# Kernel tuning notes

Hardware: AMD Instinct MI355X
Metric: run time of the kernel (lower is better)

Reference implementation:

```python
import jax, jax.numpy as jnp
import numpy as np

E = 16777216       # total edges across the batch
NG = 1024          # num_graphs
K = 32             # action_topk
TEMP = 1.0         # policy_temperature


def setup_inputs() -> dict:
    key = jax.random.key(0)
    k1, k2, k3, k4, k5 = jax.random.split(key, 5)
    edge_logits = jax.random.normal(k1, (E,), dtype=jnp.float32)
    edge_scores = jax.random.normal(k2, (E,), dtype=jnp.float32)
    stop_logits = jax.random.normal(k3, (NG,), dtype=jnp.float32)
    edge_batch = jnp.sort(jax.random.randint(k4, (E,), 0, NG)).astype(jnp.int64)
    candidate_mask = jax.random.randint(k5, (E,), 0, 2).astype(bool)
    return {
        'edge_logits': edge_logits,
        'edge_scores': edge_scores,
        'stop_logits': stop_logits,
        'edge_batch': edge_batch,
        'candidate_mask': candidate_mask,
    }


def _topk_edge_mask(edge_scores, edge_batch, candidate_mask):
    """Faithful port of _select_topk_candidate_edges, returning a boolean keep
    mask over all E edges (fixed shape; indices of kept edges are implicit)."""
    neg_inf = jnp.finfo(jnp.float32).min
    # Non-candidates get a sentinel segment NG and -inf score so they sort last.
    seg_key = jnp.where(candidate_mask, edge_batch, NG)
    score = jnp.where(candidate_mask, edge_scores.astype(jnp.float32), neg_inf)
    # Sort by score descending, then stable-sort by segment id
    order_score = jnp.argsort(-score)
    seg_by_score = seg_key[order_score]
    order_seg = jnp.argsort(seg_by_score)          # jax argsort is stable
    cand_sorted = order_score[order_seg]           # original edge ids, sorted
    seg_sorted = seg_by_score[order_seg]
    # rank within each segment = position - segment start (exclusive cumsum)
    counts = jnp.bincount(seg_sorted, length=NG + 1)
    start = jnp.concatenate([jnp.zeros((1,), counts.dtype), jnp.cumsum(counts)[:-1]])
    rank = jnp.arange(E) - start[seg_sorted]
    keep_sorted = (rank < K) & (seg_sorted < NG)
    return jnp.zeros((E,), dtype=bool).at[cand_sorted].set(keep_sorted)


def _segment_logsumexp_1d(logits, segment_ids, num_segments):
    """Faithful port of torch _segment_logsumexp_1d."""
    neg_inf = jnp.finfo(logits.dtype).min
    eps = jnp.finfo(logits.dtype).eps
    max_per = jnp.full((num_segments,), neg_inf, dtype=logits.dtype).at[segment_ids].max(logits)
    exp = jnp.exp(logits - max_per[segment_ids])
    sum_per = jnp.zeros((num_segments,), dtype=logits.dtype).at[segment_ids].add(exp)
    return jnp.log(jnp.maximum(sum_per, eps)) + max_per


def reference(edge_logits, edge_scores, stop_logits, edge_batch, candidate_mask):
    neg_inf = jnp.finfo(jnp.float32).min
    # Per-graph top-k pruning of candidate edges by edge_scores
    valid = _topk_edge_mask(edge_scores, edge_batch, candidate_mask)
    # Segmented temperature softmax over (valid edges + stop action)
    logits_t = edge_logits / TEMP
    stop_t = stop_logits / TEMP
    masked = jnp.where(valid, logits_t, neg_inf)
    lse_edges = _segment_logsumexp_1d(masked, edge_batch, NG)       # [NG]
    log_denom = jnp.logaddexp(lse_edges, stop_t)                    # [NG]
    log_prob_edge = jnp.where(valid, logits_t - log_denom[edge_batch], neg_inf)
    return log_prob_edge
```

## Files before the change

kernel.cpp:

```cpp
#include <hip/hip_runtime.h>
#include <float.h>

#define TPB  512
#define KTOP 32
#define GCAP 512
#define LCAP 1024
#define SENT_U32 0xFF7F0000u
#define VCLAMP 3.0e38f
#define STHRESH 2.0f

__device__ __forceinline__ unsigned int f2u(float f){
  unsigned int u = __float_as_uint(f);
  return (u & 0x80000000u) ? ~u : (u | 0x80000000u);
}

__device__ int suffix_total(int* hist, int NB, int* gsum, int tid){
  int GS = NB >> 8;
  if (tid < 256){
    int p = 0, base = tid * GS;
    for (int j = 0; j < GS; ++j) p += hist[base + j];
    gsum[tid] = p;
  }
  __syncthreads();
  for (int d = 1; d < 256; d <<= 1){
    int v = 0;
    if (tid < 256) v = (tid + d < 256) ? gsum[tid + d] : 0;
    __syncthreads();
    if (tid < 256) gsum[tid] += v;
    __syncthreads();
  }
  return gsum[0];
}

__device__ int find_bin(int* hist, int NB, int* gsum, int R, int* s2, int tid,
                        int* above_out){
  int GS = NB >> 8;
  if (tid < 256){
    int St  = gsum[tid];
    int St1 = (tid < 255) ? gsum[tid + 1] : 0;
    if (R > St1 && R <= St) s2[0] = tid;
  }
  __syncthreads();
  if (tid == 0){
    int G = s2[0];
    int above = (G < 255) ? gsum[G + 1] : 0;
    int b = (G + 1) * GS - 1;
    for (; b > G * GS; --b){
      int h = hist[b];
      if (above + h >= R) break;
      above += h;
    }
    s2[0] = b; s2[1] = above;
  }
  __syncthreads();
  int bin = s2[0];
  *above_out = s2[1];
  __syncthreads();
  return bin;
}

__global__ void __launch_bounds__(TPB, 4)
fused_kernel(const float* __restrict__ logits,
             const float* __restrict__ scores,
             const float* __restrict__ stop_logits,
             const int* __restrict__ batch,
             const int* __restrict__ cmask,
             float* __restrict__ out, int E, int NG)
{
  __shared__ int hist[2048];
  __shared__ int gsum[256];
  __shared__ int s2[2];
  __shared__ int sbounds[2];
  __shared__ int srch[2];
  __shared__ unsigned int st_u[LCAP];
  __shared__ int st_i[LCAP];
  __shared__ unsigned int bin_u[GCAP];
  __shared__ int bin_i[GCAP];
  __shared__ int ab_i[KTOP];
  __shared__ int vidx[KTOP];
  __shared__ float vlog[KTOP];
  __shared__ int scnt, cnt_bin, cnt_ab, vcnt;
  __shared__ float sh_logden;

  int tid = threadIdx.x;
  int g = blockIdx.x;

  {
    int grp = tid >> 8 & 1;
    int lt  = tid & 255;
    int target = g + grp;
    int lo = 0, hi = E;
    for (int round = 0; round < 3; ++round){
      if (lt == 0) srch[grp] = 0;
      __syncthreads();
      int width = hi - lo;
      int pred = 0;
      if (width > 256){
        long long w = width;
        int q = lo + (int)((w * (long long)lt) >> 8);
        pred = (batch[q] < target) ? 1 : 0;
      }
      unsigned long long bal = __ballot(pred);
      if ((tid & 63) == 0) atomicAdd(&srch[grp], __popcll(bal));
      __syncthreads();
      if (width > 256){
        long long w = width;
        int c = srch[grp];
        int nlo = (c > 0)   ? lo + (int)((w * (long long)(c - 1)) >> 8) + 1 : lo;
        int nhi = (c < 256) ? lo + (int)((w * (long long)c) >> 8)          : hi;
        lo = nlo; hi = nhi;
      }
      __syncthreads();
    }
    if (lt == 0) srch[grp] = 0;
    __syncthreads();
    int width = hi - lo;
    int pred = (lt < width) ? ((batch[lo + lt] < target) ? 1 : 0) : 0;
    unsigned long long bal = __ballot(pred);
    if ((tid & 63) == 0) atomicAdd(&srch[grp], __popcll(bal));
    __syncthreads();
    if (lt == 0) sbounds[grp] = lo + srch[grp];
  }
  if (tid == 0){ scnt = 0; cnt_bin = 0; cnt_ab = 0; vcnt = 0; }
  __syncthreads();
  int s = sbounds[0], e = sbounds[1];

  int s4 = (s + 3) & ~3; if (s4 > e) s4 = e;
  int e4 = e & ~3;       if (e4 < s4) e4 = s4;
  const float4* sc4 = (const float4*)scores;
  const float SENT = __uint_as_float(SENT_U32);
  const float4 sv = make_float4(SENT, SENT, SENT, SENT);
  float4* out4 = (float4*)out;

  auto proc4 = [&](float4 a, int bidx){
    int h = (a.x >= STHRESH ? 1 : 0) | (a.y >= STHRESH ? 2 : 0)
          | (a.z >= STHRESH ? 4 : 0) | (a.w >= STHRESH ? 8 : 0);
    if (h){
      int sl = atomicAdd(&scnt, __popc(h));
      if (h & 1){ if (sl < LCAP){ st_u[sl] = f2u(a.x); st_i[sl] = bidx;     } sl++; }
      if (h & 2){ if (sl < LCAP){ st_u[sl] = f2u(a.y); st_i[sl] = bidx + 1; } sl++; }
      if (h & 4){ if (sl < LCAP){ st_u[sl] = f2u(a.z); st_i[sl] = bidx + 2; } sl++; }
      if (h & 8){ if (sl < LCAP){ st_u[sl] = f2u(a.w); st_i[sl] = bidx + 3; } }
    }
  };
  auto st1 = [&](float sc, int idx){
    if (sc >= STHRESH){
      int sl = atomicAdd(&scnt, 1);
      if (sl < LCAP){ st_u[sl] = f2u(sc); st_i[sl] = idx; }
    }
  };
  {
    int i = s + tid;  if (i < s4){ st1(scores[i], i); out[i] = SENT; }
    int j = e4 + tid; if (j < e) { st1(scores[j], j); out[j] = SENT; }
    int q  = (s4 >> 2) + tid;
    int qe = (e4 >> 2);
    for (; q + 3 * TPB < qe; q += 4 * TPB){
      float4 a0 = sc4[q];
      float4 a1 = sc4[q +     TPB];
      float4 a2 = sc4[q + 2 * TPB];
      float4 a3 = sc4[q + 3 * TPB];
      out4[q]           = sv;
      out4[q +     TPB] = sv;
      out4[q + 2 * TPB] = sv;
      out4[q + 3 * TPB] = sv;
      proc4(a0, q << 2);
      proc4(a1, (q +     TPB) << 2);
      proc4(a2, (q + 2 * TPB) << 2);
      proc4(a3, (q + 3 * TPB) << 2);
    }
    for (; q < qe; q += TPB){
      float4 a = sc4[q];
      out4[q] = sv;
      proc4(a, q << 2);
    }
  }
  __syncthreads();

  int nst = scnt;
  bool ovf = (nst > LCAP);
  if (!ovf){
    for (int t = tid; t < nst; t += TPB){
      int idx = st_i[t];
      if (cmask[idx]){
        int sl = atomicAdd(&cnt_bin, 1);
        if (sl < GCAP){ bin_u[sl] = st_u[t]; bin_i[sl] = idx; }
      }
    }
  }
  __syncthreads();
  int S = cnt_bin;

  if (!ovf && S >= KTOP && S <= GCAP){
    for (int jj = tid; jj < S; jj += TPB){
      unsigned long long kj = ((unsigned long long)bin_u[jj] << 32)
                            | (unsigned long long)(unsigned)(~(unsigned)bin_i[jj]);
      int rank = 0;
      for (int k = 0; k < S; ++k){
        unsigned long long kk = ((unsigned long long)bin_u[k] << 32)
                              | (unsigned long long)(unsigned)(~(unsigned)bin_i[k]);
        rank += (kk > kj) ? 1 : 0;
      }
      if (rank < KTOP){
        int sl = atomicAdd(&vcnt, 1);
        if (sl < KTOP) vidx[sl] = bin_i[jj];
      }
    }
  } else {
    auto scan_sc = [&](auto&& fn){
      int i = s + tid;  if (i < s4) fn(scores[i], i);
      int j = e4 + tid; if (j < e)  fn(scores[j], j);
      for (int q = (s4 >> 2) + tid, qe = (e4 >> 2); q < qe; q += TPB){
        float4 sc = sc4[q];
        int base = q << 2;
        fn(sc.x, base);     fn(sc.y, base + 1);
        fn(sc.z, base + 2); fn(sc.w, base + 3);
      }
    };
    auto is_cand = [&](int idx) -> bool { return cmask[idx] != 0; };

    for (int b = tid; b < 2048; b += TPB) hist[b] = 0;
    if (tid == 0){ cnt_bin = 0; cnt_ab = 0; }
    __syncthreads();
    scan_sc([&](float sc, int idx){
      if (is_cand(idx)) atomicAdd(&hist[f2u(sc) >> 21], 1);
    });
    __syncthreads();
    int T = suffix_total(hist, 2048, gsum, tid);
    bool sel = (T > KTOP);
    unsigned int prefix = 0; int pshift = 32; int R = KTOP;
    if (sel){
      int above;
      int b1 = find_bin(hist, 2048, gsum, R, s2, tid, &above);
      R -= above; prefix = (unsigned)b1; pshift = 21;
      int hcnt = hist[b1];
      __syncthreads();
      if (hcnt > GCAP){
        for (int b = tid; b < 2048; b += TPB) hist[b] = 0;
        __syncthreads();
        scan_sc([&](float sc, int idx){
          unsigned u = f2u(sc);
          if ((u >> 21) == prefix && is_cand(idx))
            atomicAdd(&hist[(u >> 10) & 0x7FFu], 1);
        });
        __syncthreads();
        suffix_total(hist, 2048, gsum, tid);
        int b2 = find_bin(hist, 2048, gsum, R, s2, tid, &above);
        R -= above; prefix = (prefix << 11) | (unsigned)b2; pshift = 10;
        hcnt = hist[b2];
        __syncthreads();
        if (hcnt > GCAP){
          for (int b = tid; b < 1024; b += TPB) hist[b] = 0;
          __syncthreads();
          scan_sc([&](float sc, int idx){
            unsigned u = f2u(sc);
            if ((u >> 10) == prefix && is_cand(idx))
              atomicAdd(&hist[u & 0x3FFu], 1);
          });
          __syncthreads();
          suffix_total(hist, 1024, gsum, tid);
          int b3 = find_bin(hist, 1024, gsum, R, s2, tid, &above);
          R -= above; prefix = (prefix << 10) | (unsigned)b3; pshift = 0;
          __syncthreads();
        }
      }
      scan_sc([&](float sc, int idx){
        unsigned u = f2u(sc);
        unsigned hp = (pshift < 32) ? (u >> pshift) : 0u;
        if (hp >= prefix){
          if (is_cand(idx)){
            if (hp == prefix){
              int sl = atomicAdd(&cnt_bin, 1);
              if (sl < GCAP){ bin_u[sl] = u; bin_i[sl] = idx; }
            } else {
              int sl = atomicAdd(&cnt_ab, 1);
              if (sl < KTOP) ab_i[sl] = idx;
            }
          }
        }
      });
      __syncthreads();
      int bn = min(cnt_bin, GCAP);
      for (int jj = tid; jj < bn; jj += TPB){
        unsigned long long kj = ((unsigned long long)bin_u[jj] << 32)
                              | (unsigned long long)(unsigned)(~(unsigned)bin_i[jj]);
        int rank = 0;
        for (int k = 0; k < bn; ++k){
          unsigned long long kk2 = ((unsigned long long)bin_u[k] << 32)
                                 | (unsigned long long)(unsigned)(~(unsigned)bin_i[k]);
          rank += (kk2 > kj) ? 1 : 0;
        }
        if (rank < R){
          int sl = atomicAdd(&vcnt, 1);
          if (sl < KTOP) vidx[sl] = bin_i[jj];
        }
      }
      int na = min(cnt_ab, KTOP);
      for (int jj = tid; jj < na; jj += TPB){
        int sl = atomicAdd(&vcnt, 1);
        if (sl < KTOP) vidx[sl] = ab_i[jj];
      }
    } else {
      scan_sc([&](float sc, int idx){
        (void)sc;
        if (is_cand(idx)){
          int sl = atomicAdd(&vcnt, 1);
          if (sl < KTOP) vidx[sl] = idx;
        }
      });
    }
  }
  __syncthreads();

  int c = min(vcnt, KTOP);
  if (tid < c) vlog[tid] = logits[vidx[tid]];
  __syncthreads();
  if (tid < 64){
    float v = (tid < c) ? vlog[tid] : -FLT_MAX;
    float m = v;
    #pragma unroll
    for (int d = 32; d; d >>= 1) m = fmaxf(m, __shfl_xor(m, d));
    float ex = (tid < c) ? expf(v - m) : 0.f;
    #pragma unroll
    for (int d = 32; d; d >>= 1) ex += __shfl_xor(ex, d);
    if (tid == 0){
      float stop = stop_logits[g];
      float logden;
      if (c == 0){
        logden = stop;
      } else {
        float lse = logf(fmaxf(ex, FLT_EPSILON)) + m;
        float mx = fmaxf(lse, stop);
        float dd = fabsf(lse - stop);
        logden = mx + log1pf(expf(-dd));
      }
      sh_logden = logden;
    }
  }
  __syncthreads();

  if (tid < c){
    float val = vlog[tid] - sh_logden;
    if (!(val >= -VCLAMP)) val = -VCLAMP;
    if (val > VCLAMP)      val =  VCLAMP;
    out[vidx[tid]] = val;
  }
}

extern "C" void kernel_launch(void* const* d_in, const int* in_sizes, int n_in,
                              void* d_out, int out_size, void* d_ws, size_t ws_size,
                              hipStream_t stream){
  const float* edge_logits = (const float*)d_in[0];
  const float* edge_scores = (const float*)d_in[1];
  const float* stop_logits = (const float*)d_in[2];
  const int*   edge_batch  = (const int*)d_in[3];
  const int*   cmask       = (const int*)d_in[4];
  int E  = in_sizes[0];
  int NG = in_sizes[2];
  float* out = (float*)d_out;
  (void)d_ws; (void)ws_size;

  hipLaunchKernelGGL(fused_kernel, dim3(NG), dim3(TPB), 0, stream,
                     edge_logits, edge_scores, stop_logits, edge_batch, cmask,
                     out, E, NG);
}
```

Baseline: 237.5 us.

## Stash threshold hits in per-thread LDS slots, halve block size

Replaces the per-float4 shared atomicAdd on a global stash counter with per-thread private slot arrays in LDS, followed by a single compaction atomic per thread after the scan. Block size drops from 512 to 256 threads, and the two-group boundary binary search is adjusted to 128 lanes per group. This cuts contention on the shared-memory atomic during the streaming pass. In exchange it uses more LDS per block and has a tighter overflow cap (12 hits per thread, 512 total), which can push more blocks onto the slow multi-pass histogram fallback.

```diff
diff --git a/kernel.cpp b/kernel.cpp
--- a/kernel.cpp
+++ b/kernel.cpp
@@ -1,10 +1,10 @@
 #include <hip/hip_runtime.h>
 #include <float.h>
 
-#define TPB  512
-#define KTOP 32
-#define GCAP 512
-#define LCAP 1024
+#define TPB   256
+#define SLOTS 12
+#define KTOP  32
+#define BCAP  512
 #define SENT_U32 0xFF7F0000u
 #define VCLAMP 3.0e38f
 #define STHRESH 2.0f
@@ -59,7 +59,7 @@
   return bin;
 }
 
-__global__ void __launch_bounds__(TPB, 4)
+__global__ void __launch_bounds__(TPB)
 fused_kernel(const float* __restrict__ logits,
              const float* __restrict__ scores,
              const float* __restrict__ stop_logits,
@@ -67,27 +67,28 @@
              const int* __restrict__ cmask,
              float* __restrict__ out, int E, int NG)
 {
-  __shared__ int hist[2048];
+  __shared__ unsigned int su[TPB * SLOTS];
+  __shared__ int          si[TPB * SLOTS];
+  __shared__ unsigned int bin_u[BCAP];
+  __shared__ int          bin_i[BCAP];
   __shared__ int gsum[256];
   __shared__ int s2[2];
   __shared__ int sbounds[2];
   __shared__ int srch[2];
-  __shared__ unsigned int st_u[LCAP];
-  __shared__ int st_i[LCAP];
-  __shared__ unsigned int bin_u[GCAP];
-  __shared__ int bin_i[GCAP];
   __shared__ int ab_i[KTOP];
   __shared__ int vidx[KTOP];
   __shared__ float vlog[KTOP];
-  __shared__ int scnt, cnt_bin, cnt_ab, vcnt;
+  __shared__ int scnt, cnt2, cnt_ab, vcnt, ovfflag;
   __shared__ float sh_logden;
 
   int tid = threadIdx.x;
   int g = blockIdx.x;
 
+  if (tid == 0){ scnt = 0; cnt2 = 0; cnt_ab = 0; vcnt = 0; ovfflag = 0; }
+
   {
-    int grp = tid >> 8 & 1;
-    int lt  = tid & 255;
+    int grp = tid >> 7;
+    int lt  = tid & 127;
     int target = g + grp;
     int lo = 0, hi = E;
     for (int round = 0; round < 3; ++round){
@@ -95,19 +96,19 @@
       __syncthreads();
       int width = hi - lo;
       int pred = 0;
-      if (width > 256){
+      if (width > 128){
         long long w = width;
-        int q = lo + (int)((w * (long long)lt) >> 8);
+        int q = lo + (int)((w * (long long)lt) >> 7);
         pred = (batch[q] < target) ? 1 : 0;
       }
       unsigned long long bal = __ballot(pred);
       if ((tid & 63) == 0) atomicAdd(&srch[grp], __popcll(bal));
       __syncthreads();
-      if (width > 256){
+      if (width > 128){
         long long w = width;
         int c = srch[grp];
-        int nlo = (c > 0)   ? lo + (int)((w * (long long)(c - 1)) >> 8) + 1 : lo;
-        int nhi = (c < 256) ? lo + (int)((w * (long long)c) >> 8)          : hi;
+        int nlo = (c > 0)   ? lo + (int)((w * (long long)(c - 1)) >> 7) + 1 : lo;
+        int nhi = (c < 128) ? lo + (int)((w * (long long)c) >> 7)          : hi;
         lo = nlo; hi = nhi;
       }
       __syncthreads();
@@ -120,9 +121,8 @@
     if ((tid & 63) == 0) atomicAdd(&srch[grp], __popcll(bal));
     __syncthreads();
     if (lt == 0) sbounds[grp] = lo + srch[grp];
-  }
-  if (tid == 0){ scnt = 0; cnt_bin = 0; cnt_ab = 0; vcnt = 0; }
-  __syncthreads();
+    __syncthreads();
+  }
   int s = sbounds[0], e = sbounds[1];
 
   int s4 = (s + 3) & ~3; if (s4 > e) s4 = e;
@@ -132,26 +132,17 @@
   const float4 sv = make_float4(SENT, SENT, SENT, SENT);
   float4* out4 = (float4*)out;
 
-  auto proc4 = [&](float4 a, int bidx){
-    int h = (a.x >= STHRESH ? 1 : 0) | (a.y >= STHRESH ? 2 : 0)
-          | (a.z >= STHRESH ? 4 : 0) | (a.w >= STHRESH ? 8 : 0);
-    if (h){
-      int sl = atomicAdd(&scnt, __popc(h));
-      if (h & 1){ if (sl < LCAP){ st_u[sl] = f2u(a.x); st_i[sl] = bidx;     } sl++; }
-      if (h & 2){ if (sl < LCAP){ st_u[sl] = f2u(a.y); st_i[sl] = bidx + 1; } sl++; }
-      if (h & 4){ if (sl < LCAP){ st_u[sl] = f2u(a.z); st_i[sl] = bidx + 2; } sl++; }
-      if (h & 8){ if (sl < LCAP){ st_u[sl] = f2u(a.w); st_i[sl] = bidx + 3; } }
-    }
-  };
-  auto st1 = [&](float sc, int idx){
-    if (sc >= STHRESH){
-      int sl = atomicAdd(&scnt, 1);
-      if (sl < LCAP){ st_u[sl] = f2u(sc); st_i[sl] = idx; }
+  int cnt = 0;
+  int sbase = tid * SLOTS;
+  auto stash = [&](float v, int idx){
+    if (v >= STHRESH){
+      if (cnt < SLOTS){ su[sbase + cnt] = f2u(v); si[sbase + cnt] = idx; }
+      cnt++;
     }
   };
   {
-    int i = s + tid;  if (i < s4){ st1(scores[i], i); out[i] = SENT; }
-    int j = e4 + tid; if (j < e) { st1(scores[j], j); out[j] = SENT; }
+    int i = s + tid;  if (i < s4){ stash(scores[i], i); out[i] = SENT; }
+    int j = e4 + tid; if (j < e) { stash(scores[j], j); out[j] = SENT; }
     int q  = (s4 >> 2) + tid;
     int qe = (e4 >> 2);
     for (; q + 3 * TPB < qe; q += 4 * TPB){
@@ -163,49 +154,66 @@
       out4[q +     TPB] = sv;
       out4[q + 2 * TPB] = sv;
       out4[q + 3 * TPB] = sv;
-      proc4(a0, q << 2);
-      proc4(a1, (q +     TPB) << 2);
-      proc4(a2, (q + 2 * TPB) << 2);
-      proc4(a3, (q + 3 * TPB) << 2);
+      int b0 = q << 2, b1 = (q + TPB) << 2, b2 = (q + 2 * TPB) << 2, b3 = (q + 3 * TPB) << 2;
+      stash(a0.x, b0);     stash(a0.y, b0 + 1); stash(a0.z, b0 + 2); stash(a0.w, b0 + 3);
+      stash(a1.x, b1);     stash(a1.y, b1 + 1); stash(a1.z, b1 + 2); stash(a1.w, b1 + 3);
+      stash(a2.x, b2);     stash(a2.y, b2 + 1); stash(a2.z, b2 + 2); stash(a2.w, b2 + 3);
+      stash(a3.x, b3);     stash(a3.y, b3 + 1); stash(a3.z, b3 + 2); stash(a3.w, b3 + 3);
     }
     for (; q < qe; q += TPB){
       float4 a = sc4[q];
       out4[q] = sv;
-      proc4(a, q << 2);
-    }
-  }
-  __syncthreads();
-
-  int nst = scnt;
-  bool ovf = (nst > LCAP);
+      int b0 = q << 2;
+      stash(a.x, b0);     stash(a.y, b0 + 1);
+      stash(a.z, b0 + 2); stash(a.w, b0 + 3);
+    }
+  }
+  if (cnt > SLOTS) ovfflag = 1;
+  int myc = cnt < SLOTS ? cnt : SLOTS;
+  __syncthreads();
+  if (myc > 0){
+    int base = atomicAdd(&scnt, myc);
+    for (int k = 0; k < myc; ++k){
+      int sl = base + k;
+      if (sl < BCAP){ bin_u[sl] = su[sbase + k]; bin_i[sl] = si[sbase + k]; }
+      else ovfflag = 1;
+    }
+  }
+  __syncthreads();
+  int total = scnt; if (total > BCAP) total = BCAP;
+
+  unsigned int* sv_u = su;
+  int*          sv_i = si;
+  bool ovf = (ovfflag != 0);
   if (!ovf){
-    for (int t = tid; t < nst; t += TPB){
-      int idx = st_i[t];
+    for (int t = tid; t < total; t += TPB){
+      int idx = bin_i[t];
       if (cmask[idx]){
-        int sl = atomicAdd(&cnt_bin, 1);
-        if (sl < GCAP){ bin_u[sl] = st_u[t]; bin_i[sl] = idx; }
-      }
-    }
-  }
-  __syncthreads();
-  int S = cnt_bin;
-
-  if (!ovf && S >= KTOP && S <= GCAP){
+        int sl = atomicAdd(&cnt2, 1);
+        sv_u[sl] = bin_u[t]; sv_i[sl] = idx;
+      }
+    }
+  }
+  __syncthreads();
+  int S = cnt2;
+
+  if (!ovf && S >= KTOP){
     for (int jj = tid; jj < S; jj += TPB){
-      unsigned long long kj = ((unsigned long long)bin_u[jj] << 32)
-                            | (unsigned long long)(unsigned)(~(unsigned)bin_i[jj]);
+      unsigned long long kj = ((unsigned long long)sv_u[jj] << 32)
+                            | (unsigned long long)(unsigned)(~(unsigned)sv_i[jj]);
       int rank = 0;
       for (int k = 0; k < S; ++k){
-        unsigned long long kk = ((unsigned long long)bin_u[k] << 32)
-                              | (unsigned long long)(unsigned)(~(unsigned)bin_i[k]);
+        unsigned long long kk = ((unsigned long long)sv_u[k] << 32)
+                              | (unsigned long long)(unsigned)(~(unsigned)sv_i[k]);
         rank += (kk > kj) ? 1 : 0;
       }
       if (rank < KTOP){
         int sl = atomicAdd(&vcnt, 1);
-        if (sl < KTOP) vidx[sl] = bin_i[jj];
+        if (sl < KTOP) vidx[sl] = sv_i[jj];
       }
     }
   } else {
+    int* hist = (int*)su;
     auto scan_sc = [&](auto&& fn){
       int i = s + tid;  if (i < s4) fn(scores[i], i);
       int j = e4 + tid; if (j < e)  fn(scores[j], j);
@@ -219,7 +227,7 @@
     auto is_cand = [&](int idx) -> bool { return cmask[idx] != 0; };
 
     for (int b = tid; b < 2048; b += TPB) hist[b] = 0;
-    if (tid == 0){ cnt_bin = 0; cnt_ab = 0; }
+    if (tid == 0){ scnt = 0; cnt_ab = 0; }
     __syncthreads();
     scan_sc([&](float sc, int idx){
       if (is_cand(idx)) atomicAdd(&hist[f2u(sc) >> 21], 1);
@@ -234,7 +242,7 @@
       R -= above; prefix = (unsigned)b1; pshift = 21;
       int hcnt = hist[b1];
       __syncthreads();
-      if (hcnt > GCAP){
+      if (hcnt > BCAP){
         for (int b = tid; b < 2048; b += TPB) hist[b] = 0;
         __syncthreads();
         scan_sc([&](float sc, int idx){
@@ -248,7 +256,7 @@
         R -= above; prefix = (prefix << 11) | (unsigned)b2; pshift = 10;
         hcnt = hist[b2];
         __syncthreads();
-        if (hcnt > GCAP){
+        if (hcnt > BCAP){
           for (int b = tid; b < 1024; b += TPB) hist[b] = 0;
           __syncthreads();
           scan_sc([&](float sc, int idx){
@@ -269,8 +277,8 @@
         if (hp >= prefix){
           if (is_cand(idx)){
             if (hp == prefix){
-              int sl = atomicAdd(&cnt_bin, 1);
-              if (sl < GCAP){ bin_u[sl] = u; bin_i[sl] = idx; }
+              int sl = atomicAdd(&scnt, 1);
+              if (sl < BCAP){ bin_u[sl] = u; bin_i[sl] = idx; }
             } else {
               int sl = atomicAdd(&cnt_ab, 1);
               if (sl < KTOP) ab_i[sl] = idx;
@@ -279,7 +287,7 @@
         }
       });
       __syncthreads();
-      int bn = min(cnt_bin, GCAP);
+      int bn = min(scnt, BCAP);
       for (int jj = tid; jj < bn; jj += TPB){
         unsigned long long kj = ((unsigned long long)bin_u[jj] << 32)
                               | (unsigned long long)(unsigned)(~(unsigned)bin_i[jj]);
```

After: 236.9 us. No clear change (-0.3%).
